# Optimization experiments

Hardware: AMD Instinct MI355X
Metric: run time of the kernel (lower is better)

Reference implementation:

```python
import jax, jax.numpy as jnp
import numpy as np
from jax.scipy.special import logsumexp

B, T, N = 512, 1024, 64


def setup_inputs() -> dict:
    key = jax.random.key(0)
    k1, k2, k3, k4, k5, k6 = jax.random.split(key, 6)
    emit = jax.random.normal(k1, (B, T, N), dtype=jnp.float32)
    target = jax.random.randint(k2, (B, T), 0, N)
    # valid monotone mask: each sequence has length in [T//2, T], length >= 1
    lengths = jax.random.randint(k3, (B,), T // 2, T + 1)
    mask = jnp.arange(T)[None, :] < lengths[:, None]  # [B, T] bool
    trans = 0.1 * jax.random.normal(k4, (N, N), dtype=jnp.float32)
    strans = 0.1 * jax.random.normal(k5, (N,), dtype=jnp.float32)
    etrans = 0.1 * jax.random.normal(k6, (N,), dtype=jnp.float32)
    return {"emit": emit, "target": target, "mask": mask,
            "trans": trans, "strans": strans, "etrans": etrans}


def _get_logZ(emit_t, mask_t, trans, strans, etrans):
    # emit_t: [T, B, N], mask_t: [T, B]
    alpha0 = strans[None, :] + emit_t[0]  # [B, N]

    def step(alpha, inp):
        e_i, m_i = inp  # [B, N], [B]
        # scores[b, j] = logsumexp_i(alpha[b, i] + trans[i, j] + e_i[b, j])
        scores = logsumexp(alpha[:, :, None] + trans[None, :, :], axis=1) + e_i
        alpha = jnp.where(m_i[:, None], scores, alpha)
        return alpha, None

    alpha, _ = jax.lax.scan(step, alpha0, (emit_t[1:], mask_t[1:]))
    logZ = logsumexp(alpha + etrans[None, :], axis=1).sum()
    return logZ / B


def _get_score(emit_t, target_t, mask_t, trans, strans, etrans):
    # emit_t: [T, B, N], target_t/mask_t: [T, B]
    emit_scores = jnp.take_along_axis(emit_t, target_t[:, :, None], axis=2)[:, :, 0]  # [T, B]
    trans_scores = trans[target_t[:-1], target_t[1:]]  # [T-1, B]
    scores = emit_scores.at[1:].add(trans_scores)
    score = jnp.where(mask_t, scores, 0.0).sum()
    ends = mask_t.sum(axis=0) - 1  # [B]
    score = score + strans[target_t[0]].sum()
    last_tags = target_t[ends, jnp.arange(target_t.shape[1])]
    score = score + etrans[last_tags].sum()
    return score / B


def reference(emit, target, mask, trans, strans, etrans):
    # batch_first=True -> move to time-major [T, B, ...]
    emit_t = jnp.swapaxes(emit, 0, 1)
    target_t = target.T
    mask_t = mask.T
    logZ = _get_logZ(emit_t, mask_t, trans, strans, etrans)
    score = _get_score(emit_t, target_t, mask_t, trans, strans, etrans)
    return logZ - score
```

## Files before the change

### kernel.cpp

```cpp
#include <hip/hip_runtime.h>

#define Bn 512
#define Tn 1024
#define Nn 64
#define WB 4
#define BURN 16

typedef float    f4  __attribute__((ext_vector_type(4)));
typedef __fp16   pk2 __attribute__((ext_vector_type(2)));
typedef __fp16   pk4 __attribute__((ext_vector_type(4)));
typedef __fp16   pk8 __attribute__((ext_vector_type(8)));
typedef _Float16 h8v __attribute__((ext_vector_type(8)));

__device__ __forceinline__ float wave_sum(float v) {
#pragma unroll
    for (int off = 32; off >= 1; off >>= 1) v += __shfl_xor(v, off, 64);
    return v;
}

__global__ __launch_bounds__(64) void crf_mfma(
    const float* __restrict__ emit,
    const int*   __restrict__ target,
    const int*   __restrict__ mask,
    const float* __restrict__ trans,
    const float* __restrict__ strans,
    const float* __restrict__ etrans,
    float*       __restrict__ out)
{
    const int lane = threadIdx.x;
    const int n = lane & 15;
    const int g = lane >> 4;
    const int b = blockIdx.x & (Bn - 1);
    const int h = blockIdx.x >> 9;
    const int m = 16 * h + n;
    const size_t ebase = (size_t)b * Tn * Nn;

    h8v A[4][2];
#pragma unroll
    for (int r = 0; r < 4; ++r)
#pragma unroll
        for (int hh = 0; hh < 2; ++hh) {
            h8v a;
#pragma unroll
            for (int j = 0; j < 8; ++j) {
                int kk = 32 * hh + 16 * (j >> 2) + 4 * g + (j & 3);
                a[j] = (_Float16)__expf(trans[kk * Nn + 16 * r + n]);
            }
            A[r][hh] = a;
        }

    const int* mrow = mask + (size_t)b * Tn;
    int lsum = 0;
#pragma unroll
    for (int k = 0; k < Tn / Nn; ++k) lsum += mrow[k * Nn + lane];
#pragma unroll
    for (int off = 32; off >= 1; off >>= 1) lsum += __shfl_xor(lsum, off, 64);
    const int len = lsum;

    const int a0v   = (m * len) >> 6;
    const int a1v   = ((m + 1) * len) >> 6;
    int start = a0v - BURN; if (start < 1) start = 1;
    const int tendv = a1v - 1;
    const int maxk  = ((len + 63) >> 6) + BURN;

    float wsel[4][4];
#pragma unroll
    for (int r = 0; r < 4; ++r) {
        f4 ee = *(const f4*)(emit + ebase + (size_t)(len - 1) * Nn + 16 * r + 4 * g);
        f4 et = *(const f4*)(etrans + 16 * r + 4 * g);
#pragma unroll
        for (int c = 0; c < 4; ++c)
            wsel[r][c] = (m == 63) ? __expf(ee[c] + et[c]) : 1.0f;
    }

    float U[4][4];
#pragma unroll
    for (int r = 0; r < 4; ++r) {
        f4 st = *(const f4*)(strans + 16 * r + 4 * g);
#pragma unroll
        for (int c = 0; c < 4; ++c)
            U[r][c] = (start == 1) ? __expf(st[c]) : 1.0f;
    }

    int   S = 0;
    float L0 = 0.0f, contrib = 0.0f;

    f4 rbuf[8][4];
#pragma unroll
    for (int d = 0; d < 8; ++d) {
        int tr = start - 1 + d; if (tr > Tn - 1) tr = Tn - 1;
        const f4* p = (const f4*)(emit + ebase + (size_t)tr * Nn);
#pragma unroll
        for (int r = 0; r < 4; ++r) rbuf[d][r] = p[4 * r + g];
    }

    const f4 zero4 = {0.f, 0.f, 0.f, 0.f};
    const int nkb = (maxk + 7) >> 3;

    for (int kb = 0; kb < nkb; ++kb) {
#pragma unroll
        for (int q = 0; q < 8; ++q) {
            const int k = 8 * kb + q;

            float Wx[4][4];
#pragma unroll
            for (int r = 0; r < 4; ++r)
#pragma unroll
                for (int c = 0; c < 4; ++c) Wx[r][c] = __expf(rbuf[q][r][c]);
            {
                int tr = start + k + 7; if (tr > Tn - 1) tr = Tn - 1;
                const f4* p = (const f4*)(emit + ebase + (size_t)tr * Nn);
#pragma unroll
                for (int r = 0; r < 4; ++r) rbuf[q][r] = p[4 * r + g];
            }

            bool br = m && ((start + k) == a0v);
            if (__any(br)) {
                float cs = 0.f;
#pragma unroll
                for (int r = 0; r < 4; ++r)
#pragma unroll
                    for (int c = 0; c < 4; ++c) cs += U[r][c];
                cs += __shfl_xor(cs, 16, 64);
                cs += __shfl_xor(cs, 32, 64);
                float l0v = __logf(cs);
                if (br) { L0 = l0v; S = 0; }
            }

            float m0 = fmaxf(fmaxf(U[0][0], U[0][1]), fmaxf(U[0][2], U[0][3]));
            float m1 = fmaxf(fmaxf(U[1][0], U[1][1]), fmaxf(U[1][2], U[1][3]));
            float m2 = fmaxf(fmaxf(U[2][0], U[2][1]), fmaxf(U[2][2], U[2][3]));
            float m3 = fmaxf(fmaxf(U[3][0], U[3][1]), fmaxf(U[3][2], U[3][3]));
            float mx = fmaxf(fmaxf(m0, m1), fmaxf(m2, m3));
            mx = fmaxf(mx, __shfl_xor(mx, 16, 64));
            mx = fmaxf(mx, __shfl_xor(mx, 32, 64));
            const int mk = 127 - ((__float_as_int(mx) >> 23) & 0xff);
            S += mk;
            const float sc2 = __int_as_float((127 + mk) << 23);

            float P_[4][4];
#pragma unroll
            for (int r = 0; r < 4; ++r)
#pragma unroll
                for (int c = 0; c < 4; ++c) P_[r][c] = U[r][c] * sc2 * Wx[r][c];

            pk2 c00 = __builtin_amdgcn_cvt_pkrtz(P_[0][0], P_[0][1]);
            pk2 c01 = __builtin_amdgcn_cvt_pkrtz(P_[0][2], P_[0][3]);
            pk2 c10 = __builtin_amdgcn_cvt_pkrtz(P_[1][0], P_[1][1]);
            pk2 c11 = __builtin_amdgcn_cvt_pkrtz(P_[1][2], P_[1][3]);
            pk2 c20 = __builtin_amdgcn_cvt_pkrtz(P_[2][0], P_[2][1]);
            pk2 c21 = __builtin_amdgcn_cvt_pkrtz(P_[2][2], P_[2][3]);
            pk2 c30 = __builtin_amdgcn_cvt_pkrtz(P_[3][0], P_[3][1]);
            pk2 c31 = __builtin_amdgcn_cvt_pkrtz(P_[3][2], P_[3][3]);
            pk4 b0lo = __builtin_shufflevector(c00, c01, 0, 1, 2, 3);
            pk4 b0hi = __builtin_shufflevector(c10, c11, 0, 1, 2, 3);
            pk4 b1lo = __builtin_shufflevector(c20, c21, 0, 1, 2, 3);
            pk4 b1hi = __builtin_shufflevector(c30, c31, 0, 1, 2, 3);
            pk8 b0p = __builtin_shufflevector(b0lo, b0hi, 0, 1, 2, 3, 4, 5, 6, 7);
            pk8 b1p = __builtin_shufflevector(b1lo, b1hi, 0, 1, 2, 3, 4, 5, 6, 7);
            h8v B0 = __builtin_bit_cast(h8v, b0p);
            h8v B1 = __builtin_bit_cast(h8v, b1p);

#pragma unroll
            for (int r = 0; r < 4; ++r) {
                f4 acc = __builtin_amdgcn_mfma_f32_16x16x32_f16(A[r][0], B0, zero4, 0, 0, 0);
                acc     = __builtin_amdgcn_mfma_f32_16x16x32_f16(A[r][1], B1, acc,   0, 0, 0);
#pragma unroll
                for (int c = 0; c < 4; ++c) U[r][c] = acc[c];
            }

            bool rec = (start + k) == tendv;
            if (__any(rec)) {
                float cs = 0.f;
#pragma unroll
                for (int r = 0; r < 4; ++r)
#pragma unroll
                    for (int c = 0; c < 4; ++c) cs = fmaf(U[r][c], wsel[r][c], cs);
                cs += __shfl_xor(cs, 16, 64);
                cs += __shfl_xor(cs, 32, 64);
                float lv = __logf(cs);
                if (rec) contrib = lv - (float)S * 0.6931471805599453f - L0;
            }
        }
    }

    float tot = wave_sum(contrib) * 0.25f;

    float sc = 0.0f;
    const int* trow = target + (size_t)b * Tn;
    if (h == 0) {
#pragma unroll
        for (int k = 0; k < Tn / Nn; ++k) {
            int t = k * Nn + lane;
            if (t < len) {
                int gT = trow[t];
                sc += emit[ebase + (size_t)t * Nn + gT];
                if (t > 0) sc += trans[trow[t - 1] * Nn + gT];
            }
        }
        sc = wave_sum(sc);
    }

    if (lane == 0) {
        float add = tot;
        if (h == 0) add -= sc + strans[trow[0]] + etrans[trow[len - 1]];
        atomicAdd(out, add * (1.0f / (float)Bn));
    }
}

extern "C" void kernel_launch(void* const* d_in, const int* in_sizes, int n_in,
                              void* d_out, int out_size, void* d_ws, size_t ws_size,
                              hipStream_t stream) {
    const float* emit   = (const float*)d_in[0];
    const int*   target = (const int*)d_in[1];
    const int*   mask   = (const int*)d_in[2];
    const float* trans  = (const float*)d_in[3];
    const float* strans = (const float*)d_in[4];
    const float* etrans = (const float*)d_in[5];
    float* out = (float*)d_out;

    (void)hipMemsetAsync(out, 0, sizeof(float), stream);
    crf_mfma<<<Bn * WB, Nn, 0, stream>>>(emit, target, mask, trans, strans, etrans, out);
}
```

Baseline: 238.0 us.

## Stage emission rows through LDS with async global_load_lds ring buffer

Replaces the 8-deep register ring of prefetched emission rows with a 4-slot LDS ring. Each slot is filled by asynchronous global-to-LDS loads issued three steps ahead, gated by explicit vmcnt waits. The goal is to free the many VGPRs the register prefetch ring occupied and to keep loads overlapped with the serial MFMA recurrence. In exchange it adds 16 KB of LDS per block, an LDS read each step, redundant per-lane loads, and a shallower prefetch distance.

```diff
diff --git a/kernel.cpp b/kernel.cpp
--- a/kernel.cpp
+++ b/kernel.cpp
@@ -5,12 +5,23 @@
 #define Nn 64
 #define WB 4
 #define BURN 16
+#define NBUF 4
 
 typedef float    f4  __attribute__((ext_vector_type(4)));
 typedef __fp16   pk2 __attribute__((ext_vector_type(2)));
 typedef __fp16   pk4 __attribute__((ext_vector_type(4)));
 typedef __fp16   pk8 __attribute__((ext_vector_type(8)));
 typedef _Float16 h8v __attribute__((ext_vector_type(8)));
+
+typedef __attribute__((address_space(1))) void as1_void;
+typedef __attribute__((address_space(3))) void as3_void;
+
+__device__ __forceinline__ void stage16(const float* g, float* l) {
+    __builtin_amdgcn_global_load_lds((as1_void*)(unsigned long long)g,
+                                     (as3_void*)(unsigned long long)l, 16, 0, 0);
+}
+
+#define VMCNT(N) asm volatile("s_waitcnt vmcnt(" #N ")" ::: "memory")
 
 __device__ __forceinline__ float wave_sum(float v) {
 #pragma unroll
@@ -27,6 +38,8 @@
     const float* __restrict__ etrans,
     float*       __restrict__ out)
 {
+    __shared__ __align__(16) float sbuf[NBUF * 1024];
+
     const int lane = threadIdx.x;
     const int n = lane & 15;
     const int g = lane >> 4;
@@ -85,33 +98,42 @@
     int   S = 0;
     float L0 = 0.0f, contrib = 0.0f;
 
-    f4 rbuf[8][4];
-#pragma unroll
-    for (int d = 0; d < 8; ++d) {
-        int tr = start - 1 + d; if (tr > Tn - 1) tr = Tn - 1;
-        const f4* p = (const f4*)(emit + ebase + (size_t)tr * Nn);
-#pragma unroll
-        for (int r = 0; r < 4; ++r) rbuf[d][r] = p[4 * r + g];
-    }
+    auto stage = [&](int bf, int kstep) {
+        int tr = start + kstep - 1; if (tr > Tn - 1) tr = Tn - 1;
+        const float* gs = emit + ebase + (size_t)tr * Nn + 4 * g;
+        float* ls = sbuf + bf * 1024;
+#pragma unroll
+        for (int r = 0; r < 4; ++r)
+            stage16(gs + 16 * r, ls + 256 * r);
+    };
+
+    VMCNT(0);
+    stage(0, 0); stage(1, 1); stage(2, 2);
 
     const f4 zero4 = {0.f, 0.f, 0.f, 0.f};
-    const int nkb = (maxk + 7) >> 3;
+    const int nkb = (maxk + 3) >> 2;
 
     for (int kb = 0; kb < nkb; ++kb) {
 #pragma unroll
-        for (int q = 0; q < 8; ++q) {
-            const int k = 8 * kb + q;
-
+        for (int q = 0; q < 4; ++q) {
+            const int k = 4 * kb + q;
+
+            stage((q + 3) & 3, k + 3);
+            VMCNT(12);
+            __builtin_amdgcn_sched_barrier(0);
+
+            const float* sb = sbuf + q * 1024 + 64 * g + 4 * n;
+            f4 w0 = *(const f4*)(sb);
+            f4 w1 = *(const f4*)(sb + 256);
+            f4 w2 = *(const f4*)(sb + 512);
+            f4 w3 = *(const f4*)(sb + 768);
             float Wx[4][4];
 #pragma unroll
-            for (int r = 0; r < 4; ++r)
-#pragma unroll
-                for (int c = 0; c < 4; ++c) Wx[r][c] = __expf(rbuf[q][r][c]);
-            {
-                int tr = start + k + 7; if (tr > Tn - 1) tr = Tn - 1;
-                const f4* p = (const f4*)(emit + ebase + (size_t)tr * Nn);
-#pragma unroll
-                for (int r = 0; r < 4; ++r) rbuf[q][r] = p[4 * r + g];
+            for (int c = 0; c < 4; ++c) {
+                Wx[0][c] = __expf(w0[c]);
+                Wx[1][c] = __expf(w1[c]);
+                Wx[2][c] = __expf(w2[c]);
+                Wx[3][c] = __expf(w3[c]);
             }
 
             bool br = m && ((start + k) == a0v);
@@ -183,6 +205,7 @@
             }
         }
     }
+    VMCNT(0);
 
     float tot = wave_sum(contrib) * 0.25f;
 
```

New measurement: 228.2 us. 1.04x faster.
